# Performance work log

Measured on AMD Instinct MI355X. Metric: run time of the kernel, lower is better.

The kernel has to match this reference:

```python
import jax, jax.numpy as jnp
import numpy as np

B, T, T3, P = 512, 128, 64, 12
IN1, H1 = 64, 256
IN2, H2 = 64, 256
IN3, H3 = 32, 128
GLOB, OUT = 32, 2
FC_IN = 2 * H1 + H2 + GLOB + 2 * P * H3  # 3872


def lstm_last(x, Wih, Whh, bih, bhh):
    """Single-layer batch-first LSTM (PyTorch gate order i,f,g,o); returns last hidden state [B,H]."""
    Bx = x.shape[0]
    H = Whh.shape[1]
    # precompute input projections for all timesteps: [T, B, 4H]
    xg = jnp.swapaxes(jnp.einsum('bti,gi->btg', x, Wih) + bih + bhh, 0, 1)

    def step(carry, g):
        h, c = carry
        gates = g + h @ Whh.T
        i, f, gg, o = jnp.split(gates, 4, axis=-1)
        c = jax.nn.sigmoid(f) * c + jax.nn.sigmoid(i) * jnp.tanh(gg)
        h = jax.nn.sigmoid(o) * jnp.tanh(c)
        return (h, c), None

    h0 = jnp.zeros((Bx, H), x.dtype)
    (h, _), _ = jax.lax.scan(step, (h0, h0), xg)
    return h


def setup_inputs() -> dict:
    key = jax.random.key(0)
    ks = jax.random.split(key, 20)
    n = lambda k, s: jax.random.normal(k, s, dtype=jnp.float32)
    w = lambda k, s: jax.random.normal(k, s, dtype=jnp.float32) * 0.05
    return {
        'current_game': n(ks[0], (B, GLOB)),
        'games_home': n(ks[1], (B, T, IN1)),
        'games_away': n(ks[2], (B, T, IN1)),
        'games_vs': n(ks[3], (B, T, IN2)),
        'players_home': n(ks[4], (B, P, T3, IN3)),
        'players_away': n(ks[5], (B, P, T3, IN3)),
        'Wih1': w(ks[6], (4 * H1, IN1)), 'Whh1': w(ks[7], (4 * H1, H1)),
        'bih1': w(ks[8], (4 * H1,)), 'bhh1': w(ks[9], (4 * H1,)),
        'Wih2': w(ks[10], (4 * H2, IN2)), 'Whh2': w(ks[11], (4 * H2, H2)),
        'bih2': w(ks[12], (4 * H2,)), 'bhh2': w(ks[13], (4 * H2,)),
        'Wih3': w(ks[14], (4 * H3, IN3)), 'Whh3': w(ks[15], (4 * H3, H3)),
        'bih3': w(ks[16], (4 * H3,)), 'bhh3': w(ks[17], (4 * H3,)),
        'Wfc': w(ks[18], (OUT, FC_IN)), 'bfc': w(ks[19], (OUT,)),
    }


def reference(current_game, games_home, games_away, games_vs, players_home, players_away,
              Wih1, Whh1, bih1, bhh1, Wih2, Whh2, bih2, bhh2, Wih3, Whh3, bih3, bhh3,
              Wfc, bfc):
    h_home = lstm_last(games_home, Wih1, Whh1, bih1, bhh1)   # [B, H1]
    h_away = lstm_last(games_away, Wih1, Whh1, bih1, bhh1)   # shared rnn weights
    h_vs = lstm_last(games_vs, Wih2, Whh2, bih2, bhh2)       # [B, H2]

    def players_feat(xp):
        # fold the player dim into batch: one batched LSTM pass instead of P launches
        b, p = xp.shape[0], xp.shape[1]
        h = lstm_last(xp.reshape(b * p, xp.shape[2], xp.shape[3]), Wih3, Whh3, bih3, bhh3)
        return h.reshape(b, p * H3)  # concat in player order, matching the torch loop

    feat = jnp.concatenate([
        h_home, h_away, h_vs,
        players_feat(players_home), players_feat(players_away),
        current_game,
    ], axis=1)  # [B, FC_IN]
    return feat @ Wfc.T + bfc
```

## Files before the change

kernel.cpp:

```cpp
#include <hip/hip_runtime.h>
#include <stdint.h>

typedef __bf16 bf16;
typedef bf16 bf16x8 __attribute__((ext_vector_type(8)));
typedef bf16 bf16x4 __attribute__((ext_vector_type(4)));
typedef float f32x4 __attribute__((ext_vector_type(4)));

#define DEV __device__ __forceinline__

static const size_t OFF_W1 = 0;
static const size_t OFF_W2 = OFF_W1 + (size_t)640 * 1024;
static const size_t OFF_W3 = OFF_W2 + (size_t)640 * 1024;
static const size_t OFF_B1 = OFF_W3 + (size_t)160 * 1024;
static const size_t OFF_B2 = OFF_B1 + 4096;
static const size_t OFF_B3 = OFF_B2 + 4096;
static const size_t OFF_FEAT = OFF_B3 + 2048;
static const size_t WS_NEEDED = OFF_FEAT + (size_t)512 * 3840 * 4;

DEV float sigm(float x) { return 1.f / (1.f + __expf(-x)); }
DEV float tanh_(float x) { return 1.f - 2.f / (__expf(2.f * x) + 1.f); }

template <int H, int IN, int NT, int NKT>
DEV void packW(const float* __restrict__ Wih, const float* __restrict__ Whh,
               bf16* __restrict__ dst, int i) {
  int e = i & 7, lane = (i >> 3) & 63;
  int rest = i >> 9;
  int kt = rest % NKT; rest /= NKT;
  int nt = rest % NT;  int w = rest / NT;
  int quad = lane >> 4, l16 = lane & 15;
  constexpr int NTG = NT / 4, UW = NT * 4;
  int unit = w * UW + (nt % NTG) * 16 + l16;
  int g = nt / NTG;
  int r = g * H + unit;
  int k = kt * 32 + quad * 8 + e;
  float v = (k < IN) ? Wih[r * IN + k] : Whh[r * H + (k - IN)];
  dst[i] = (bf16)v;
}

__global__ void prep_kernel(const float* __restrict__ Wih1, const float* __restrict__ Whh1,
                            const float* __restrict__ bih1, const float* __restrict__ bhh1,
                            const float* __restrict__ Wih2, const float* __restrict__ Whh2,
                            const float* __restrict__ bih2, const float* __restrict__ bhh2,
                            const float* __restrict__ Wih3, const float* __restrict__ Whh3,
                            const float* __restrict__ bih3, const float* __restrict__ bhh3,
                            uint8_t* __restrict__ ws) {
  const int gt = blockIdx.x * blockDim.x + threadIdx.x;
  const int gs = gridDim.x * blockDim.x;
  bf16* W1 = (bf16*)(ws + OFF_W1);
  bf16* W2 = (bf16*)(ws + OFF_W2);
  bf16* W3 = (bf16*)(ws + OFF_W3);
  float* B1 = (float*)(ws + OFF_B1);
  float* B2 = (float*)(ws + OFF_B2);
  float* B3 = (float*)(ws + OFF_B3);
  for (int i = gt; i < 640 * 512; i += gs) {
    packW<256, 64, 16, 10>(Wih1, Whh1, W1, i);
    packW<256, 64, 16, 10>(Wih2, Whh2, W2, i);
  }
  for (int i = gt; i < 160 * 512; i += gs) packW<128, 32, 8, 5>(Wih3, Whh3, W3, i);
  for (int i = gt; i < 1024; i += gs) { B1[i] = bih1[i] + bhh1[i]; B2[i] = bih2[i] + bhh2[i]; }
  for (int i = gt; i < 512; i += gs) B3[i] = bih3[i] + bhh3[i];
}

template <int BM, int IN, int H, int T, int NT, int NKT, int NV, int NL, int NS, int DOM>
DEV void lstm_tile2(const float* __restrict__ x0, const float* __restrict__ x1, int halfM,
                    const bf16* __restrict__ Wd, const float* __restrict__ bsum,
                    float* __restrict__ feat, int mg, uint8_t* smem) {
  static_assert(NV + NL + NS == NT, "split");
  static_assert(NL <= 1, "NL 0/1 only");
  constexpr int MT = BM / 16;
  constexpr int NTG = NT / 4;
  constexpr int UW = NT * 4;
  constexpr int KCH = (IN + H) / 8;
  constexpr int SROW = KCH + 1;
  constexpr int AROWE = SROW * 8;
  constexpr int NF4 = BM * IN / 4;
  constexpr int XPT = NF4 / 256;

  const int tid = threadIdx.x;
  const int lane = tid & 63;
  const int w = tid >> 6;
  const int quad = lane >> 4;
  const int l16 = lane & 15;
  const int rowbase = mg * BM;

  bf16* A = (bf16*)smem;
  bf16* Wshm = (bf16*)(smem + 21504);

  const float* xb = (rowbase < halfM) ? x0 : x1;
  const int rowoff = rowbase - ((rowbase < halfM) ? 0 : halfM);

  {
    constexpr int HCH = KCH - IN / 8;
    for (int i = tid; i < BM * HCH * 4; i += 256) {
      int row = i / (HCH * 4), rem = i % (HCH * 4);
      int chunk = IN / 8 + rem / 4, d = rem % 4;
      ((uint32_t*)A)[row * SROW * 4 + chunk * 4 + d] = 0;
    }
  }
  if constexpr (NL > 0) {
    for (int idx = tid; idx < 4 * NL * NKT * 64; idx += 256) {
      int ln = idx & 63;
      int kt = (idx >> 6) % NKT;
      int rest = (idx >> 6) / NKT;
      int nl = rest % NL, w2 = rest / NL;
      int blob = (w2 * NT + NV + nl) * NKT + kt;
      *(bf16x8*)(Wshm + (size_t)((w2 * NL + nl) * NKT + kt) * 512 + ln * 8) =
          *(const bf16x8*)(Wd + (size_t)blob * 512 + ln * 8);
    }
  }
  bf16x8 wreg[NV][NKT];
  {
    const bf16* Wv = Wd + (size_t)(w * NT) * NKT * 512 + lane * 8;
#pragma unroll
    for (int nt = 0; nt < NV; ++nt)
#pragma unroll
      for (int kt = 0; kt < NKT; ++kt)
        wreg[nt][kt] = *(const bf16x8*)(Wv + (size_t)(nt * NKT + kt) * 512);
  }
  const bf16* Wstream = Wd + (size_t)(w * NT + NV + NL) * NKT * 512 + lane * 8;

  float bias[4][NTG];
#pragma unroll
  for (int g = 0; g < 4; ++g)
#pragma unroll
    for (int ut = 0; ut < NTG; ++ut)
      bias[g][ut] = bsum[g * H + w * UW + ut * 16 + l16];

  bf16x8 sbuf[2][NS > 0 ? NS : 1];
  if constexpr (NS > 0) {
#pragma unroll
    for (int ns = 0; ns < NS; ++ns)
      sbuf[0][ns] = *(const bf16x8*)(Wstream + (size_t)(ns * NKT) * 512);
  }
  bf16x8 wldsbuf[2];

  float4 xr[XPT];
#pragma unroll
  for (int i = 0; i < XPT; ++i) {
    int idx = i * 256 + tid;
    int row = idx / (IN / 4), c4 = idx % (IN / 4);
    xr[i] = *(const float4*)(xb + (size_t)(rowoff + row) * T * IN + c4 * 4);
  }
#pragma unroll
  for (int i = 0; i < XPT; ++i) {
    int idx = i * 256 + tid;
    int row = idx / (IN / 4), c4 = idx % (IN / 4);
    int k = c4 * 4;
    bf16x4 p;
    p[0] = (bf16)xr[i].x; p[1] = (bf16)xr[i].y; p[2] = (bf16)xr[i].z; p[3] = (bf16)xr[i].w;
    *(bf16x4*)(A + row * AROWE + (k >> 3) * 8 + (k & 7)) = p;
  }
  __syncthreads();
  if constexpr (NL > 0)
    wldsbuf[0] = *(const bf16x8*)(Wshm + (size_t)(w * NKT) * 512 + lane * 8);

  float c[MT * NTG * 4];
#pragma unroll
  for (int i = 0; i < MT * NTG * 4; ++i) c[i] = 0.f;

  f32x4 acc[NT][MT];
  bf16x8 afbuf[2][MT];

#pragma unroll 1
  for (int t = 0; t < T; ++t) {
#pragma unroll
    for (int nt = 0; nt < NT; ++nt)
#pragma unroll
      for (int mt = 0; mt < MT; ++mt) acc[nt][mt] = f32x4{0.f, 0.f, 0.f, 0.f};
#pragma unroll
    for (int mt = 0; mt < MT; ++mt)
      afbuf[0][mt] = *(const bf16x8*)(A + (mt * 16 + l16) * AROWE + quad * 8);
    if (t < T - 1) {
#pragma unroll
      for (int i = 0; i < XPT; ++i) {
        int idx = i * 256 + tid;
        int row = idx / (IN / 4), c4 = idx % (IN / 4);
        xr[i] = *(const float4*)(xb + (size_t)(rowoff + row) * T * IN + (size_t)(t + 1) * IN + c4 * 4);
      }
    }
#pragma unroll
    for (int kt = 0; kt < NKT; ++kt) {
      const int ktn = (kt + 1) % NKT;
      const int pc = kt & 1, pn = (kt + 1) & 1;
      if (kt + 1 < NKT) {
#pragma unroll
        for (int mt = 0; mt < MT; ++mt)
          afbuf[pn][mt] =
              *(const bf16x8*)(A + (mt * 16 + l16) * AROWE + ((kt + 1) * 4 + quad) * 8);
      }
      if constexpr (NS > 0) {
#pragma unroll
        for (int ns = 0; ns < NS; ++ns)
          sbuf[pn][ns] = *(const bf16x8*)(Wstream + (size_t)(ns * NKT + ktn) * 512);
      }
      if constexpr (NL > 0)
        wldsbuf[pn] = *(const bf16x8*)(Wshm + (size_t)(w * NKT + ktn) * 512 + lane * 8);
#pragma unroll
      for (int nt = 0; nt < NV; ++nt)
#pragma unroll
        for (int mt = 0; mt < MT; ++mt)
          acc[nt][mt] =
              __builtin_amdgcn_mfma_f32_16x16x32_bf16(afbuf[pc][mt], wreg[nt][kt], acc[nt][mt], 0, 0, 0);
      if constexpr (NL > 0) {
#pragma unroll
        for (int mt = 0; mt < MT; ++mt)
          acc[NV][mt] =
              __builtin_amdgcn_mfma_f32_16x16x32_bf16(afbuf[pc][mt], wldsbuf[pc], acc[NV][mt], 0, 0, 0);
      }
      if constexpr (NS > 0) {
#pragma unroll
        for (int ns = 0; ns < NS; ++ns)
#pragma unroll
          for (int mt = 0; mt < MT; ++mt)
            acc[NV + NL + ns][mt] = __builtin_amdgcn_mfma_f32_16x16x32_bf16(
                afbuf[pc][mt], sbuf[pc][ns], acc[NV + NL + ns][mt], 0, 0, 0);
      }
    }
    __syncthreads();

#pragma unroll
    for (int mt = 0; mt < MT; ++mt)
#pragma unroll
      for (int ut = 0; ut < NTG; ++ut)
#pragma unroll
        for (int j = 0; j < 4; ++j) {
          float gi = acc[0 * NTG + ut][mt][j] + bias[0][ut];
          float gf = acc[1 * NTG + ut][mt][j] + bias[1][ut];
          float gg = acc[2 * NTG + ut][mt][j] + bias[2][ut];
          float go = acc[3 * NTG + ut][mt][j] + bias[3][ut];
          int ci = (mt * NTG + ut) * 4 + j;
          float cc = sigm(gf) * c[ci] + sigm(gi) * tanh_(gg);
          c[ci] = cc;
          float hv = sigm(go) * tanh_(cc);
          int row = mt * 16 + quad * 4 + j;
          if (t < T - 1) {
            int k = IN + w * UW + ut * 16 + l16;
            A[row * AROWE + (k >> 3) * 8 + (k & 7)] = (bf16)hv;
          } else {
            int R = rowbase + row;
            int unit = w * UW + ut * 16 + l16;
            int b, col;
            if (DOM == 0) {
              if (R < 512) { b = R; col = unit; }
              else         { b = R - 512; col = 256 + unit; }
            } else if (DOM == 1) {
              b = R; col = 512 + unit;
            } else {
              int rr = R; int base = 768;
              if (rr >= 6144) { rr -= 6144; base = 2304; }
              b = rr / 12; int p = rr - b * 12;
              col = base + p * 128 + unit;
            }
            feat[(size_t)b * 3840 + col] = hv;
          }
        }
    if (t < T - 1) {
#pragma unroll
      for (int i = 0; i < XPT; ++i) {
        int idx = i * 256 + tid;
        int row = idx / (IN / 4), c4 = idx % (IN / 4);
        int k = c4 * 4;
        bf16x4 p;
        p[0] = (bf16)xr[i].x; p[1] = (bf16)xr[i].y; p[2] = (bf16)xr[i].z; p[3] = (bf16)xr[i].w;
        *(bf16x4*)(A + row * AROWE + (k >> 3) * 8 + (k & 7)) = p;
      }
    }
    __syncthreads();
  }
}

__global__ __launch_bounds__(256, 1) void lstm_main(const float* __restrict__ gh,
                                                    const float* __restrict__ ga,
                                                    const float* __restrict__ gv,
                                                    const float* __restrict__ ph,
                                                    const float* __restrict__ pa,
                                                    uint8_t* __restrict__ ws) {
  __shared__ uint4 smem_[62464 / 16];
  uint8_t* smem = (uint8_t*)smem_;
  float* feat = (float*)(ws + OFF_FEAT);
  int bid = blockIdx.x;
  if (bid < 64) {
    lstm_tile2<16, 64, 256, 128, 16, 10, 6, 1, 9, 0>(
        gh, ga, 512, (const bf16*)(ws + OFF_W1), (const float*)(ws + OFF_B1), feat, bid, smem);
  } else if (bid < 96) {
    lstm_tile2<16, 64, 256, 128, 16, 10, 6, 1, 9, 1>(
        gv, gv, 512, (const bf16*)(ws + OFF_W2), (const float*)(ws + OFF_B2), feat, bid - 64, smem);
  } else {
    lstm_tile2<64, 32, 128, 64, 8, 5, 8, 0, 0, 2>(
        ph, pa, 6144, (const bf16*)(ws + OFF_W3), (const float*)(ws + OFF_B3), feat, bid - 96, smem);
  }
}

__global__ void fc_kernel(const float* __restrict__ feat, const float* __restrict__ cg,
                          const float* __restrict__ Wfc, const float* __restrict__ bfc,
                          float* __restrict__ out) {
  int b = blockIdx.x, tid = threadIdx.x;
  float a0 = 0.f, a1 = 0.f;
  for (int c = tid; c < 3840; c += 256) {
    float f = feat[(size_t)b * 3840 + c];
    a0 += f * Wfc[c];
    a1 += f * Wfc[3872 + c];
  }
  if (tid < 32) {
    float f = cg[b * 32 + tid];
    a0 += f * Wfc[3840 + tid];
    a1 += f * Wfc[3872 + 3840 + tid];
  }
#pragma unroll
  for (int o = 32; o > 0; o >>= 1) {
    a0 += __shfl_down(a0, o);
    a1 += __shfl_down(a1, o);
  }
  __shared__ float red[8];
  int wv = tid >> 6;
  if ((tid & 63) == 0) { red[wv * 2] = a0; red[wv * 2 + 1] = a1; }
  __syncthreads();
  if (tid == 0) {
    out[b * 2 + 0] = red[0] + red[2] + red[4] + red[6] + bfc[0];
    out[b * 2 + 1] = red[1] + red[3] + red[5] + red[7] + bfc[1];
  }
}

extern "C" void kernel_launch(void* const* d_in, const int* in_sizes, int n_in, void* d_out,
                              int out_size, void* d_ws, size_t ws_size, hipStream_t stream) {
  const float* cg = (const float*)d_in[0];
  const float* gh = (const float*)d_in[1];
  const float* ga = (const float*)d_in[2];
  const float* gv = (const float*)d_in[3];
  const float* ph = (const float*)d_in[4];
  const float* pa = (const float*)d_in[5];
  const float* Wih1 = (const float*)d_in[6];
  const float* Whh1 = (const float*)d_in[7];
  const float* bih1 = (const float*)d_in[8];
  const float* bhh1 = (const float*)d_in[9];
  const float* Wih2 = (const float*)d_in[10];
  const float* Whh2 = (const float*)d_in[11];
  const float* bih2 = (const float*)d_in[12];
  const float* bhh2 = (const float*)d_in[13];
  const float* Wih3 = (const float*)d_in[14];
  const float* Whh3 = (const float*)d_in[15];
  const float* bih3 = (const float*)d_in[16];
  const float* bhh3 = (const float*)d_in[17];
  const float* Wfc = (const float*)d_in[18];
  const float* bfc = (const float*)d_in[19];
  uint8_t* ws = (uint8_t*)d_ws;
  if (ws_size < WS_NEEDED) return;

  hipLaunchKernelGGL(prep_kernel, dim3(512), dim3(256), 0, stream, Wih1, Whh1, bih1, bhh1,
                     Wih2, Whh2, bih2, bhh2, Wih3, Whh3, bih3, bhh3, ws);
  hipLaunchKernelGGL(lstm_main, dim3(288), dim3(256), 0, stream, gh, ga, gv, ph, pa, ws);
  hipLaunchKernelGGL(fc_kernel, dim3(512), dim3(256), 0, stream,
                     (const float*)(ws + OFF_FEAT), cg, Wfc, bfc, (float*)d_out);
}
```

Measured before the change: 2.129 ms.

## Split resident LSTM weights across VGPRs and AGPRs, move more into LDS

Resident recurrent weight fragments are split between VGPRs and AGPRs, using inline-asm MFMA with an AGPR B operand. This lets more weights stay on-chip instead of being streamed from global memory every timestep. On devices that allow about 90 KB of dynamic shared memory, two weight tiles per wave go to LDS instead of one, with a fallback kernel otherwise. It also moves accumulator zeroing to the end of each step and adds s_nops after the barrier for MFMA hazards. The inline asm bypasses compiler hazard tracking, and a larger LDS footprint is only safe because there is one block per CU.

```diff
diff --git a/kernel.cpp b/kernel.cpp
--- a/kernel.cpp
+++ b/kernel.cpp
@@ -5,6 +5,7 @@
 typedef bf16 bf16x8 __attribute__((ext_vector_type(8)));
 typedef bf16 bf16x4 __attribute__((ext_vector_type(4)));
 typedef float f32x4 __attribute__((ext_vector_type(4)));
+typedef int i32x4 __attribute__((ext_vector_type(4)));
 
 #define DEV __device__ __forceinline__
 
@@ -19,6 +20,13 @@
 
 DEV float sigm(float x) { return 1.f / (1.f + __expf(-x)); }
 DEV float tanh_(float x) { return 1.f - 2.f / (__expf(2.f * x) + 1.f); }
+
+DEV void mfma_bv(f32x4& acc, i32x4 a, i32x4 b) {
+  asm("v_mfma_f32_16x16x32_bf16 %0, %1, %2, %0" : "+a"(acc) : "v"(a), "v"(b));
+}
+DEV void mfma_ba(f32x4& acc, i32x4 a, i32x4 b) {
+  asm("v_mfma_f32_16x16x32_bf16 %0, %1, %2, %0" : "+a"(acc) : "v"(a), "a"(b));
+}
 
 template <int H, int IN, int NT, int NKT>
 DEV void packW(const float* __restrict__ Wih, const float* __restrict__ Whh,
@@ -61,20 +69,20 @@
   for (int i = gt; i < 512; i += gs) B3[i] = bih3[i] + bhh3[i];
 }
 
-template <int BM, int IN, int H, int T, int NT, int NKT, int NV, int NL, int NS, int DOM>
-DEV void lstm_tile2(const float* __restrict__ x0, const float* __restrict__ x1, int halfM,
+template <int BM, int IN, int H, int T, int NT, int NKT, int NVV, int NVA, int NL, int NS,
+          int DOM>
+DEV void lstm_tile3(const float* __restrict__ x0, const float* __restrict__ x1, int halfM,
                     const bf16* __restrict__ Wd, const float* __restrict__ bsum,
                     float* __restrict__ feat, int mg, uint8_t* smem) {
-  static_assert(NV + NL + NS == NT, "split");
-  static_assert(NL <= 1, "NL 0/1 only");
+  static_assert(NVV + NVA + NL + NS == NT, "split");
+  static_assert((NL == 0 && NS == 0) || (NKT % 2 == 0), "wrap parity");
   constexpr int MT = BM / 16;
   constexpr int NTG = NT / 4;
   constexpr int UW = NT * 4;
   constexpr int KCH = (IN + H) / 8;
   constexpr int SROW = KCH + 1;
   constexpr int AROWE = SROW * 8;
-  constexpr int NF4 = BM * IN / 4;
-  constexpr int XPT = NF4 / 256;
+  constexpr int XPT = BM * IN / 4 / 256;
 
   const int tid = threadIdx.x;
   const int lane = tid & 63;
@@ -84,7 +92,7 @@
   const int rowbase = mg * BM;
 
   bf16* A = (bf16*)smem;
-  bf16* Wshm = (bf16*)(smem + 21504);
+  bf16* Wshm = (bf16*)(smem + (size_t)BM * AROWE * 2);
 
   const float* xb = (rowbase < halfM) ? x0 : x1;
   const int rowoff = rowbase - ((rowbase < halfM) ? 0 : halfM);
@@ -103,21 +111,30 @@
       int kt = (idx >> 6) % NKT;
       int rest = (idx >> 6) / NKT;
       int nl = rest % NL, w2 = rest / NL;
-      int blob = (w2 * NT + NV + nl) * NKT + kt;
+      int blob = (w2 * NT + NVV + NVA + nl) * NKT + kt;
       *(bf16x8*)(Wshm + (size_t)((w2 * NL + nl) * NKT + kt) * 512 + ln * 8) =
           *(const bf16x8*)(Wd + (size_t)blob * 512 + ln * 8);
     }
   }
-  bf16x8 wreg[NV][NKT];
+  i32x4 wregv[NVV > 0 ? NVV : 1][NKT];
   {
     const bf16* Wv = Wd + (size_t)(w * NT) * NKT * 512 + lane * 8;
 #pragma unroll
-    for (int nt = 0; nt < NV; ++nt)
+    for (int nt = 0; nt < NVV; ++nt)
 #pragma unroll
       for (int kt = 0; kt < NKT; ++kt)
-        wreg[nt][kt] = *(const bf16x8*)(Wv + (size_t)(nt * NKT + kt) * 512);
-  }
-  const bf16* Wstream = Wd + (size_t)(w * NT + NV + NL) * NKT * 512 + lane * 8;
+        wregv[nt][kt] = *(const i32x4*)(Wv + (size_t)(nt * NKT + kt) * 512);
+  }
+  i32x4 wrega[NVA > 0 ? NVA : 1][NKT];
+  {
+    const bf16* Wa = Wd + (size_t)(w * NT + NVV) * NKT * 512 + lane * 8;
+#pragma unroll
+    for (int nt = 0; nt < NVA; ++nt)
+#pragma unroll
+      for (int kt = 0; kt < NKT; ++kt)
+        wrega[nt][kt] = *(const i32x4*)(Wa + (size_t)(nt * NKT + kt) * 512);
+  }
+  const bf16* Wstream = Wd + (size_t)(w * NT + NVV + NVA + NL) * NKT * 512 + lane * 8;
 
   float bias[4][NTG];
 #pragma unroll
@@ -126,13 +143,8 @@
     for (int ut = 0; ut < NTG; ++ut)
       bias[g][ut] = bsum[g * H + w * UW + ut * 16 + l16];
 
-  bf16x8 sbuf[2][NS > 0 ? NS : 1];
-  if constexpr (NS > 0) {
-#pragma unroll
-    for (int ns = 0; ns < NS; ++ns)
-      sbuf[0][ns] = *(const bf16x8*)(Wstream + (size_t)(ns * NKT) * 512);
-  }
-  bf16x8 wldsbuf[2];
+  i32x4 sbuf[2][NS > 0 ? NS : 1];
+  i32x4 wlds[2][NL > 0 ? NL : 1];
 
   float4 xr[XPT];
 #pragma unroll
@@ -151,31 +163,41 @@
     *(bf16x4*)(A + row * AROWE + (k >> 3) * 8 + (k & 7)) = p;
   }
   __syncthreads();
-  if constexpr (NL > 0)
-    wldsbuf[0] = *(const bf16x8*)(Wshm + (size_t)(w * NKT) * 512 + lane * 8);
+  if constexpr (NS > 0) {
+#pragma unroll
+    for (int ns = 0; ns < NS; ++ns)
+      sbuf[0][ns] = *(const i32x4*)(Wstream + (size_t)(ns * NKT) * 512);
+  }
+  if constexpr (NL > 0) {
+#pragma unroll
+    for (int nl = 0; nl < NL; ++nl)
+      wlds[0][nl] = *(const i32x4*)(Wshm + (size_t)((w * NL + nl) * NKT) * 512 + lane * 8);
+  }
 
   float c[MT * NTG * 4];
 #pragma unroll
   for (int i = 0; i < MT * NTG * 4; ++i) c[i] = 0.f;
 
   f32x4 acc[NT][MT];
-  bf16x8 afbuf[2][MT];
+#pragma unroll
+  for (int nt = 0; nt < NT; ++nt)
+#pragma unroll
+    for (int mt = 0; mt < MT; ++mt) acc[nt][mt] = f32x4{0.f, 0.f, 0.f, 0.f};
+
+  i32x4 afbuf[2][MT];
 
 #pragma unroll 1
   for (int t = 0; t < T; ++t) {
 #pragma unroll
-    for (int nt = 0; nt < NT; ++nt)
-#pragma unroll
-      for (int mt = 0; mt < MT; ++mt) acc[nt][mt] = f32x4{0.f, 0.f, 0.f, 0.f};
-#pragma unroll
     for (int mt = 0; mt < MT; ++mt)
-      afbuf[0][mt] = *(const bf16x8*)(A + (mt * 16 + l16) * AROWE + quad * 8);
+      afbuf[0][mt] = *(const i32x4*)(A + (mt * 16 + l16) * AROWE + quad * 8);
     if (t < T - 1) {
 #pragma unroll
       for (int i = 0; i < XPT; ++i) {
         int idx = i * 256 + tid;
         int row = idx / (IN / 4), c4 = idx % (IN / 4);
-        xr[i] = *(const float4*)(xb + (size_t)(rowoff + row) * T * IN + (size_t)(t + 1) * IN + c4 * 4);
+        xr[i] =
+            *(const float4*)(xb + (size_t)(rowoff + row) * T * IN + (size_t)(t + 1) * IN + c4 * 4);
       }
     }
 #pragma unroll
@@ -185,38 +207,43 @@
       if (kt + 1 < NKT) {
 #pragma unroll
         for (int mt = 0; mt < MT; ++mt)
-          afbuf[pn][mt] =
-              *(const bf16x8*)(A + (mt * 16 + l16) * AROWE + ((kt + 1) * 4 + quad) * 8);
+          afbuf[pn][mt] = *(const i32x4*)(A + (mt * 16 + l16) * AROWE + ((kt + 1) * 4 + quad) * 8);
       }
       if constexpr (NS > 0) {
 #pragma unroll
         for (int ns = 0; ns < NS; ++ns)
-          sbuf[pn][ns] = *(const bf16x8*)(Wstream + (size_t)(ns * NKT + ktn) * 512);
-      }
-      if constexpr (NL > 0)
-        wldsbuf[pn] = *(const bf16x8*)(Wshm + (size_t)(w * NKT + ktn) * 512 + lane * 8);
-#pragma unroll
-      for (int nt = 0; nt < NV; ++nt)
-#pragma unroll
-        for (int mt = 0; mt < MT; ++mt)
-          acc[nt][mt] =
-              __builtin_amdgcn_mfma_f32_16x16x32_bf16(afbuf[pc][mt], wreg[nt][kt], acc[nt][mt], 0, 0, 0);
+          sbuf[pn][ns] = *(const i32x4*)(Wstream + (size_t)(ns * NKT + ktn) * 512);
+      }
       if constexpr (NL > 0) {
 #pragma unroll
-        for (int mt = 0; mt < MT; ++mt)
-          acc[NV][mt] =
-              __builtin_amdgcn_mfma_f32_16x16x32_bf16(afbuf[pc][mt], wldsbuf[pc], acc[NV][mt], 0, 0, 0);
+        for (int nl = 0; nl < NL; ++nl)
+          wlds[pn][nl] = *(const i32x4*)(Wshm + (size_t)((w * NL + nl) * NKT + ktn) * 512 + lane * 8);
+      }
+#pragma unroll
+      for (int nt = 0; nt < NVV; ++nt)
+#pragma unroll
+        for (int mt = 0; mt < MT; ++mt) mfma_bv(acc[nt][mt], afbuf[pc][mt], wregv[nt][kt]);
+#pragma unroll
+      for (int nt = 0; nt < NVA; ++nt)
+#pragma unroll
+        for (int mt = 0; mt < MT; ++mt) mfma_ba(acc[NVV + nt][mt], afbuf[pc][mt], wrega[nt][kt]);
+      if constexpr (NL > 0) {
+#pragma unroll
+        for (int nl = 0; nl < NL; ++nl)
+#pragma unroll
+          for (int mt = 0; mt < MT; ++mt)
+            mfma_bv(acc[NVV + NVA + nl][mt], afbuf[pc][mt], wlds[pc][nl]);
       }
       if constexpr (NS > 0) {
 #pragma unroll
         for (int ns = 0; ns < NS; ++ns)
 #pragma unroll
           for (int mt = 0; mt < MT; ++mt)
-            acc[NV + NL + ns][mt] = __builtin_amdgcn_mfma_f32_16x16x32_bf16(
-                afbuf[pc][mt], sbuf[pc][ns], acc[NV + NL + ns][mt], 0, 0, 0);
+            mfma_bv(acc[NVV + NVA + NL + ns][mt], afbuf[pc][mt], sbuf[pc][ns]);
       }
     }
     __syncthreads();
+    asm volatile("s_nop 7\n\ts_nop 7\n\ts_nop 7" ::);
 
 #pragma unroll
     for (int mt = 0; mt < MT; ++mt)
@@ -254,6 +281,10 @@
             feat[(size_t)b * 3840 + col] = hv;
           }
         }
+#pragma unroll
+    for (int nt = 0; nt < NT; ++nt)
+#pragma unroll
+      for (int mt = 0; mt < MT; ++mt) acc[nt][mt] = f32x4{0.f, 0.f, 0.f, 0.f};
     if (t < T - 1) {
 #pragma unroll
       for (int i = 0; i < XPT; ++i) {
@@ -269,26 +300,41 @@
   }
 }
 
-__global__ __launch_bounds__(256, 1) void lstm_main(const float* __restrict__ gh,
-                                                    const float* __restrict__ ga,
-                                                    const float* __restrict__ gv,
-                                                    const float* __restrict__ ph,
-                                                    const float* __restrict__ pa,
-                                                    uint8_t* __restrict__ ws) {
-  __shared__ uint4 smem_[62464 / 16];
-  uint8_t* smem = (uint8_t*)smem_;
+template <int NL1, int NS1>
+DEV void lstm_body(const float* gh, const float* ga, const float* gv, const float* ph,
+                   const float* pa, uint8_t* ws, uint8_t* smem) {
   float* feat = (float*)(ws + OFF_FEAT);
   int bid = blockIdx.x;
   if (bid < 64) {
-    lstm_tile2<16, 64, 256, 128, 16, 10, 6, 1, 9, 0>(
+    lstm_tile3<16, 64, 256, 128, 16, 10, 2, 4, NL1, NS1, 0>(
         gh, ga, 512, (const bf16*)(ws + OFF_W1), (const float*)(ws + OFF_B1), feat, bid, smem);
   } else if (bid < 96) {
-    lstm_tile2<16, 64, 256, 128, 16, 10, 6, 1, 9, 1>(
+    lstm_tile3<16, 64, 256, 128, 16, 10, 2, 4, NL1, NS1, 1>(
         gv, gv, 512, (const bf16*)(ws + OFF_W2), (const float*)(ws + OFF_B2), feat, bid - 64, smem);
   } else {
-    lstm_tile2<64, 32, 128, 64, 8, 5, 8, 0, 0, 2>(
+    lstm_tile3<64, 32, 128, 64, 8, 5, 3, 5, 0, 0, 2>(
         ph, pa, 6144, (const bf16*)(ws + OFF_W3), (const float*)(ws + OFF_B3), feat, bid - 96, smem);
   }
+}
+
+__global__ __launch_bounds__(256, 1) void lstm_main_big(const float* __restrict__ gh,
+                                                        const float* __restrict__ ga,
+                                                        const float* __restrict__ gv,
+                                                        const float* __restrict__ ph,
+                                                        const float* __restrict__ pa,
+                                                        uint8_t* __restrict__ ws) {
+  extern __shared__ uint8_t smem[];
+  lstm_body<2, 8>(gh, ga, gv, ph, pa, ws, smem);
+}
+
+__global__ __launch_bounds__(256, 1) void lstm_main_small(const float* __restrict__ gh,
+                                                          const float* __restrict__ ga,
+                                                          const float* __restrict__ gv,
+                                                          const float* __restrict__ ph,
+                                                          const float* __restrict__ pa,
+                                                          uint8_t* __restrict__ ws) {
+  extern __shared__ uint8_t smem[];
+  lstm_body<1, 9>(gh, ga, gv, ph, pa, ws, smem);
 }
 
 __global__ void fc_kernel(const float* __restrict__ feat, const float* __restrict__ cg,
@@ -348,7 +394,18 @@
 
   hipLaunchKernelGGL(prep_kernel, dim3(512), dim3(256), 0, stream, Wih1, Whh1, bih1, bhh1,
                      Wih2, Whh2, bih2, bhh2, Wih3, Whh3, bih3, bhh3, ws);
-  hipLaunchKernelGGL(lstm_main, dim3(288), dim3(256), 0, stream, gh, ga, gv, ph, pa, ws);
+
+  int dev = 0, maxShm = 0;
+  (void)hipGetDevice(&dev);
+  (void)hipDeviceGetAttribute(&maxShm, hipDeviceAttributeMaxSharedMemoryPerBlock, dev);
+  hipError_t ae = hipFuncSetAttribute((const void*)lstm_main_big,
+                                      hipFuncAttributeMaxDynamicSharedMemorySize, 92416);
+  if (ae == hipSuccess && maxShm >= 92416) {
+    hipLaunchKernelGGL(lstm_main_big, dim3(288), dim3(256), 92416, stream, gh, ga, gv, ph, pa, ws);
+  } else {
+    hipLaunchKernelGGL(lstm_main_small, dim3(288), dim3(256), 51456, stream, gh, ga, gv, ph, pa,
+                       ws);
+  }
   hipLaunchKernelGGL(fc_kernel, dim3(512), dim3(256), 0, stream,
                      (const float*)(ws + OFF_FEAT), cg, Wfc, bfc, (float*)d_out);
 }
```

After: 1.928 ms. 1.1x faster.
